# Kernel optimization log

Hardware: AMD Instinct MI355X
Metric: run time of the kernel (lower is better)

Reference implementation:

```python
import jax, jax.numpy as jnp
import numpy as np

M_NODES, N_FEAT, HIDDEN = 1024, 64, 64


def _linear_init(key, fan_in, fan_out):
    kw, kb = jax.random.split(key)
    s = 1.0 / np.sqrt(fan_in)
    W = jax.random.uniform(kw, (fan_in, fan_out), minval=-s, maxval=s, dtype=jnp.float32)
    b = jax.random.uniform(kb, (fan_out,), minval=-s, maxval=s, dtype=jnp.float32)
    return W, b


def setup_inputs() -> dict:
    key = jax.random.key(0)
    ks = jax.random.split(key, 9)
    M, n, hid = M_NODES, N_FEAT, HIDDEN
    We1, be1 = _linear_init(ks[0], 2 * n + 2, hid)  # phi_e layer 1: [h_i, h_j, d2, a]
    We2, be2 = _linear_init(ks[1], hid, hid)         # phi_e layer 2
    Wx1, bx1 = _linear_init(ks[2], hid, hid)         # phi_x layer 1
    Wx2, bx2 = _linear_init(ks[3], hid, 1)           # phi_x layer 2 (scalar edge weight)
    Wh1, bh1 = _linear_init(ks[4], n + hid, hid)     # phi_h layer 1: [h_i, m_i]
    Wh2, bh2 = _linear_init(ks[5], hid, n)           # phi_h layer 2
    x = jax.random.normal(ks[6], (M, 3), dtype=jnp.float32)
    a = jax.random.uniform(ks[7], (M, M, 1), dtype=jnp.float32)
    h = jax.random.normal(ks[8], (M, n), dtype=jnp.float32)  # embedding table (all node ids)
    return dict(x=x, a=a, h=h, We1=We1, be1=be1, We2=We2, be2=be2,
                Wx1=Wx1, bx1=bx1, Wx2=Wx2, bx2=bx2, Wh1=Wh1, bh1=bh1, Wh2=Wh2, bh2=bh2)


def reference(x, a, h, We1, be1, We2, be2, Wx1, bx1, Wx2, bx2, Wh1, bh1, Wh2, bh2):
    M = x.shape[0]
    n = h.shape[1]
    C = 1.0 / (M - 1)
    # pairwise coordinate differences and squared distances
    diff = x[:, None, :] - x[None, :, :]                 # [M, M, 3]
    d2 = jnp.sum(diff * diff, axis=-1, keepdims=True)    # [M, M, 1]
    # phi_e layer-1 computed without materializing the [M, M, 2n+2] concat:
    # split We1 rows for h_i, h_j, d2, a contributions
    pe_i = h @ We1[:n]           # [M, hid]
    pe_j = h @ We1[n:2 * n]      # [M, hid]
    pre = pe_i[:, None, :] + pe_j[None, :, :] + d2 * We1[2 * n] + a * We1[2 * n + 1] + be1
    m = jax.nn.silu(jax.nn.silu(pre) @ We2 + be2)        # [M, M, hid]
    # coordinate update: x_i' = x_i + C * sum_j (x_i - x_j) * phi_x(m_ij)
    s = jax.nn.silu(m @ Wx1 + bx1) @ Wx2 + bx2           # [M, M, 1]
    mask = (1.0 - jnp.eye(M, dtype=x.dtype))[:, :, None]  # exclude self-loops
    x_new = x + C * jnp.sum(diff * s * mask, axis=1)      # [M, 3]
    # message aggregation over complete graph minus self-loops (m_ij @ all_neighbors)
    m_i = jnp.sum(m * mask, axis=1)                      # [M, hid]
    # node update: h' = phi_h([h_i, m_i])
    h_new = jax.nn.silu(jnp.concatenate([h, m_i], axis=-1) @ Wh1 + bh1) @ Wh2 + bh2
    return x_new, h_new
```

## Files before the change

### kernel.cpp

```cpp
#include <hip/hip_runtime.h>


#define MM 1024

typedef _Float16 half8 __attribute__((ext_vector_type(8)));
typedef float f32x4 __attribute__((ext_vector_type(4)));
typedef int int4t __attribute__((ext_vector_type(4)));

__device__ __forceinline__ float fsilu(float v) {
    float e = __expf(-v);
    return v * __builtin_amdgcn_rcpf(1.0f + e);
}

__global__ void __launch_bounds__(256) egnn_prepack(
    const float* __restrict__ h, const float* __restrict__ We1,
    const float* __restrict__ be1, const float* __restrict__ We2,
    const float* __restrict__ Wx1,
    float* __restrict__ peib, float* __restrict__ pej,
    _Float16* __restrict__ we2hi, _Float16* __restrict__ we2lo,
    _Float16* __restrict__ wx1h)
{
    const int b = blockIdx.x;
    if (b < 256) {
        const int i = b * 4 + (threadIdx.x >> 6);
        const int c = threadIdx.x & 63;
        float acc1 = be1[c], acc2 = 0.0f;
        const float* __restrict__ hrow = h + i * 64;
#pragma unroll 8
        for (int cp = 0; cp < 64; ++cp) {
            const float hv = hrow[cp];
            acc1 = fmaf(hv, We1[cp * 64 + c], acc1);
            acc2 = fmaf(hv, We1[(64 + cp) * 64 + c], acc2);
        }
        peib[i * 64 + c] = acc1;
        pej[i * 64 + c]  = acc2;
    } else {
        const int idx = (b - 256) * 256 + threadIdx.x;
        const int e = idx & 7, l = (idx >> 3) & 63, f = (idx >> 9) & 7;
        const int n = f >> 1, s = f & 1;
        const int outc = 16 * n + (l & 15);
        const int kc   = 32 * s + ((l >> 4) * 8) + e;
        if (idx < 4096) {
            const float wv = We2[kc * 64 + outc];
            const _Float16 hi = (_Float16)wv;
            we2hi[idx] = hi;
            we2lo[idx] = (_Float16)(wv - (float)hi);
        } else {
            const float wv = Wx1[kc * 64 + outc];
            wx1h[idx - 4096] = (_Float16)wv;
        }
    }
}

__global__ void __launch_bounds__(256, 2) egnn_main(
    const float* __restrict__ x, const float* __restrict__ a,
    const float* __restrict__ h, const float* __restrict__ We1,
    const float* __restrict__ peib, const float* __restrict__ pej,
    const _Float16* __restrict__ we2hi, const _Float16* __restrict__ we2lo,
    const _Float16* __restrict__ wx1h,
    const float* __restrict__ be2,
    const float* __restrict__ bx1, const float* __restrict__ Wx2,
    const float* __restrict__ bx2,
    const float* __restrict__ Wh1, const float* __restrict__ bh1,
    const float* __restrict__ Wh2, const float* __restrict__ bh2,
    float* __restrict__ out)
{
    const int i = blockIdx.x;
    const int tid = threadIdx.x;
    const int w = tid >> 6;
    const int l = tid & 63;
    const int g = l >> 4;
    const int q15 = l & 15;

    __shared__ __align__(16) float peibL[64], wd2L[64], waL[64], be2L[64], bx1L[64], wx2L[64];
    __shared__ __align__(16) float partialL[256];
    __shared__ float xpartL[4][3];
    __shared__ float miL[64], hrowL[64], hid1L[64];

    if (tid < 64) {
        peibL[tid] = peib[i * 64 + tid];
        wd2L[tid]  = We1[128 * 64 + tid];
        waL[tid]   = We1[129 * 64 + tid];
        be2L[tid]  = be2[tid];
        bx1L[tid]  = bx1[tid];
        wx2L[tid]  = Wx2[tid];
        hrowL[tid] = h[i * 64 + tid];
    }
    __syncthreads();

    const half8* __restrict__ w2h = (const half8*)we2hi;
    const half8* __restrict__ w2l = (const half8*)we2lo;
    const half8* __restrict__ wxh = (const half8*)wx1h;
    half8 whi[4][2], wlo[4][2], wx1f[4][2];
#pragma unroll
    for (int n = 0; n < 4; ++n)
#pragma unroll
        for (int s = 0; s < 2; ++s) {
            whi[n][s]  = w2h[(n * 2 + s) * 64 + l];
            wlo[n][s]  = w2l[(n * 2 + s) * 64 + l];
            wx1f[n][s] = wxh[(n * 2 + s) * 64 + l];
        }

    const float xi0 = x[i * 3 + 0], xi1 = x[i * 3 + 1], xi2 = x[i * 3 + 2];
    const float bx2v = bx2[0];
    const int sl_lo = q15 + 16 * (2 * (g & 1));
    const int sl_hi = sl_lo + 16;
    const bool hiSel = (g >= 2);

    float msum[4][4];
#pragma unroll
    for (int n = 0; n < 4; ++n)
#pragma unroll
        for (int r = 0; r < 4; ++r) msum[n][r] = 0.0f;
    float xa0 = 0.0f, xa1 = 0.0f, xa2 = 0.0f;

    for (int t = 0; t < 16; ++t) {
        const int jw = t * 64 + 16 * w + q15;
        const float xj0 = x[jw * 3 + 0], xj1 = x[jw * 3 + 1], xj2 = x[jw * 3 + 2];
        const float d0 = xi0 - xj0, d1 = xi1 - xj1, d2v = xi2 - xj2;
        const float dd = fmaf(d0, d0, fmaf(d1, d1, d2v * d2v));
        const float av = a[i * MM + jw];
        const float selfmul = (jw == i) ? 0.0f : 1.0f;

        half8 P[2];
        const float* __restrict__ pejrow = pej + jw * 64;
#pragma unroll
        for (int s = 0; s < 2; ++s) {
            const f32x4 pj0 = *(const f32x4*)(pejrow + 32 * s + 8 * g);
            const f32x4 pj1 = *(const f32x4*)(pejrow + 32 * s + 8 * g + 4);
            const f32x4 pe0 = *(const f32x4*)&peibL[32 * s + 8 * g];
            const f32x4 pe1 = *(const f32x4*)&peibL[32 * s + 8 * g + 4];
            const f32x4 wd0 = *(const f32x4*)&wd2L[32 * s + 8 * g];
            const f32x4 wd1 = *(const f32x4*)&wd2L[32 * s + 8 * g + 4];
            const f32x4 wa0 = *(const f32x4*)&waL[32 * s + 8 * g];
            const f32x4 wa1 = *(const f32x4*)&waL[32 * s + 8 * g + 4];
#pragma unroll
            for (int e = 0; e < 8; ++e) {
                const float pjv = (e < 4) ? pj0[e] : pj1[e - 4];
                const float pev = (e < 4) ? pe0[e] : pe1[e - 4];
                const float wdv = (e < 4) ? wd0[e] : wd1[e - 4];
                const float wav = (e < 4) ? wa0[e] : wa1[e - 4];
                float pre = pev + pjv;
                pre = fmaf(dd, wdv, pre);
                pre = fmaf(av, wav, pre);
                P[s][e] = (_Float16)fsilu(pre);
            }
        }

        f32x4 acc1[4];
#pragma unroll
        for (int n = 0; n < 4; ++n) acc1[n] = *(const f32x4*)&be2L[16 * n + 4 * g];
#pragma unroll
        for (int n = 0; n < 4; ++n) {
            acc1[n] = __builtin_amdgcn_mfma_f32_16x16x32_f16(whi[n][0], P[0], acc1[n], 0, 0, 0);
            acc1[n] = __builtin_amdgcn_mfma_f32_16x16x32_f16(whi[n][1], P[1], acc1[n], 0, 0, 0);
            acc1[n] = __builtin_amdgcn_mfma_f32_16x16x32_f16(wlo[n][0], P[0], acc1[n], 0, 0, 0);
            acc1[n] = __builtin_amdgcn_mfma_f32_16x16x32_f16(wlo[n][1], P[1], acc1[n], 0, 0, 0);
        }

        float mf[4][4];
        int srcp[4][2];
#pragma unroll
        for (int n = 0; n < 4; ++n) {
#pragma unroll
            for (int r = 0; r < 4; ++r) {
                mf[n][r] = fsilu(acc1[n][r]);
                msum[n][r] = fmaf(mf[n][r], selfmul, msum[n][r]);
            }
            srcp[n][0] = __builtin_bit_cast(int, __builtin_amdgcn_cvt_pkrtz(mf[n][0], mf[n][1]));
            srcp[n][1] = __builtin_bit_cast(int, __builtin_amdgcn_cvt_pkrtz(mf[n][2], mf[n][3]));
        }

        half8 B2[2];
#pragma unroll
        for (int s2 = 0; s2 < 2; ++s2) {
            int4t bi;
#pragma unroll
            for (int p = 0; p < 4; ++p) {
                const int sl = (p < 2) ? sl_lo : sl_hi;
                const int va = __shfl(srcp[2 * s2][p & 1], sl, 64);
                const int vb = __shfl(srcp[2 * s2 + 1][p & 1], sl, 64);
                bi[p] = hiSel ? vb : va;
            }
            B2[s2] = __builtin_bit_cast(half8, bi);
        }

        f32x4 acc2[4];
#pragma unroll
        for (int n = 0; n < 4; ++n) acc2[n] = *(const f32x4*)&bx1L[16 * n + 4 * g];
#pragma unroll
        for (int n = 0; n < 4; ++n) {
            acc2[n] = __builtin_amdgcn_mfma_f32_16x16x32_f16(wx1f[n][0], B2[0], acc2[n], 0, 0, 0);
            acc2[n] = __builtin_amdgcn_mfma_f32_16x16x32_f16(wx1f[n][1], B2[1], acc2[n], 0, 0, 0);
        }

        float sp = 0.0f;
#pragma unroll
        for (int n = 0; n < 4; ++n) {
            const f32x4 wq = *(const f32x4*)&wx2L[16 * n + 4 * g];
#pragma unroll
            for (int r = 0; r < 4; ++r) sp = fmaf(fsilu(acc2[n][r]), wq[r], sp);
        }
        sp += __shfl_xor(sp, 16, 64);
        sp += __shfl_xor(sp, 32, 64);
        const float sv = sp + bx2v;
        xa0 = fmaf(d0, sv, xa0);
        xa1 = fmaf(d1, sv, xa1);
        xa2 = fmaf(d2v, sv, xa2);
    }

#pragma unroll
    for (int n = 0; n < 4; ++n)
#pragma unroll
        for (int r = 0; r < 4; ++r) {
            float v = msum[n][r];
            v += __shfl_xor(v, 1, 64);
            v += __shfl_xor(v, 2, 64);
            v += __shfl_xor(v, 4, 64);
            v += __shfl_xor(v, 8, 64);
            msum[n][r] = v;
        }
    if (q15 == 0) {
#pragma unroll
        for (int n = 0; n < 4; ++n) {
            f32x4 sv4;
            sv4[0] = msum[n][0]; sv4[1] = msum[n][1];
            sv4[2] = msum[n][2]; sv4[3] = msum[n][3];
            *(f32x4*)&partialL[w * 64 + 16 * n + 4 * g] = sv4;
        }
    }
    {
        float v0 = xa0, v1 = xa1, v2 = xa2;
        for (int sft = 1; sft < 64; sft <<= 1) {
            v0 += __shfl_xor(v0, sft, 64);
            v1 += __shfl_xor(v1, sft, 64);
            v2 += __shfl_xor(v2, sft, 64);
        }
        if (l == 0) { xpartL[w][0] = v0; xpartL[w][1] = v1; xpartL[w][2] = v2; }
    }
    __syncthreads();

    if (tid < 64)
        miL[tid] = partialL[tid] + partialL[64 + tid] + partialL[128 + tid] + partialL[192 + tid];
    __syncthreads();

    if (tid < 64) {
        const int kk = tid;
        float a0 = bh1[kk], a1 = 0.0f;
#pragma unroll 8
        for (int c = 0; c < 64; ++c) {
            a0 = fmaf(hrowL[c], Wh1[c * 64 + kk], a0);
            a1 = fmaf(miL[c], Wh1[(64 + c) * 64 + kk], a1);
        }
        hid1L[kk] = fsilu(a0 + a1);
    }
    __syncthreads();

    if (tid < 64) {
        float accv = bh2[tid];
#pragma unroll 8
        for (int kk = 0; kk < 64; ++kk) accv = fmaf(hid1L[kk], Wh2[kk * 64 + tid], accv);
        out[3072 + i * 64 + tid] = accv;
    }
    if (tid == 0) {
        const float C = 0.25f / 1023.0f;
        out[i * 3 + 0] = xi0 + C * (xpartL[0][0] + xpartL[1][0] + xpartL[2][0] + xpartL[3][0]);
        out[i * 3 + 1] = xi1 + C * (xpartL[0][1] + xpartL[1][1] + xpartL[2][1] + xpartL[3][1]);
        out[i * 3 + 2] = xi2 + C * (xpartL[0][2] + xpartL[1][2] + xpartL[2][2] + xpartL[3][2]);
    }
}

extern "C" void kernel_launch(void* const* d_in, const int* in_sizes, int n_in,
                              void* d_out, int out_size, void* d_ws, size_t ws_size,
                              hipStream_t stream) {
    const float* x   = (const float*)d_in[0];
    const float* a   = (const float*)d_in[1];
    const float* h   = (const float*)d_in[2];
    const float* We1 = (const float*)d_in[3];
    const float* be1 = (const float*)d_in[4];
    const float* We2 = (const float*)d_in[5];
    const float* be2 = (const float*)d_in[6];
    const float* Wx1 = (const float*)d_in[7];
    const float* bx1 = (const float*)d_in[8];
    const float* Wx2 = (const float*)d_in[9];
    const float* bx2 = (const float*)d_in[10];
    const float* Wh1 = (const float*)d_in[11];
    const float* bh1 = (const float*)d_in[12];
    const float* Wh2 = (const float*)d_in[13];
    const float* bh2 = (const float*)d_in[14];
    float* out = (float*)d_out;

    float* peib = (float*)d_ws;
    float* pej  = peib + 65536;
    _Float16* we2hi = (_Float16*)(pej + 65536);
    _Float16* we2lo = we2hi + 4096;
    _Float16* wx1h  = we2lo + 4096;

    egnn_prepack<<<dim3(288), dim3(256), 0, stream>>>(
        h, We1, be1, We2, Wx1, peib, pej, we2hi, we2lo, wx1h);
    egnn_main<<<dim3(1024), dim3(256), 0, stream>>>(
        x, a, h, We1, peib, pej, we2hi, we2lo, wx1h,
        be2, bx1, Wx2, bx2, Wh1, bh1, Wh2, bh2, out);
}
```

Measured before the change: 177.7 us.

## Move MFMA weight fragments to LDS, raise occupancy, software-prefetch pej rows

The main kernel now stages the fp16 weight fragments (We2 hi/lo and Wx1) and the row of `a` in shared memory instead of holding 24 half8 registers per lane. This frees registers so launch bounds can request 4 blocks per CU instead of 2. The j-loop is restructured into a double-buffered prefetch of pej rows and x coordinates to hide global latency. The prepack kernel is reshaped to 64-thread blocks with h rows cached in LDS. The cost is extra LDS reads before every MFMA and more shared memory per block, which may itself limit occupancy.

New measurement: 477.6 us. 169% more time.

```diff
diff --git a/kernel.cpp b/kernel.cpp
--- a/kernel.cpp
+++ b/kernel.cpp
@@ -12,7 +12,7 @@
     return v * __builtin_amdgcn_rcpf(1.0f + e);
 }
 
-__global__ void __launch_bounds__(256) egnn_prepack(
+__global__ void __launch_bounds__(64) egnn_prepack(
     const float* __restrict__ h, const float* __restrict__ We1,
     const float* __restrict__ be1, const float* __restrict__ We2,
     const float* __restrict__ Wx1,
@@ -21,11 +21,14 @@
     _Float16* __restrict__ wx1h)
 {
     const int b = blockIdx.x;
-    if (b < 256) {
-        const int i = b * 4 + (threadIdx.x >> 6);
-        const int c = threadIdx.x & 63;
+    const int tid = threadIdx.x;
+    if (b < 1024) {
+        const int i = b;
+        const int c = tid;
+        __shared__ float hrow[64];
+        hrow[c] = h[i * 64 + c];
+        __syncthreads();
         float acc1 = be1[c], acc2 = 0.0f;
-        const float* __restrict__ hrow = h + i * 64;
 #pragma unroll 8
         for (int cp = 0; cp < 64; ++cp) {
             const float hv = hrow[cp];
@@ -35,7 +38,7 @@
         peib[i * 64 + c] = acc1;
         pej[i * 64 + c]  = acc2;
     } else {
-        const int idx = (b - 256) * 256 + threadIdx.x;
+        const int idx = (b - 1024) * 64 + tid;
         const int e = idx & 7, l = (idx >> 3) & 63, f = (idx >> 9) & 7;
         const int n = f >> 1, s = f & 1;
         const int outc = 16 * n + (l & 15);
@@ -46,13 +49,12 @@
             we2hi[idx] = hi;
             we2lo[idx] = (_Float16)(wv - (float)hi);
         } else {
-            const float wv = Wx1[kc * 64 + outc];
-            wx1h[idx - 4096] = (_Float16)wv;
+            wx1h[idx - 4096] = (_Float16)Wx1[kc * 64 + outc];
         }
     }
 }
 
-__global__ void __launch_bounds__(256, 2) egnn_main(
+__global__ void __launch_bounds__(256, 4) egnn_main(
     const float* __restrict__ x, const float* __restrict__ a,
     const float* __restrict__ h, const float* __restrict__ We1,
     const float* __restrict__ peib, const float* __restrict__ pej,
@@ -72,11 +74,20 @@
     const int g = l >> 4;
     const int q15 = l & 15;
 
+    __shared__ half8 wLDS[1536];
+    __shared__ __align__(16) float aL[1024];
     __shared__ __align__(16) float peibL[64], wd2L[64], waL[64], be2L[64], bx1L[64], wx2L[64];
     __shared__ __align__(16) float partialL[256];
     __shared__ float xpartL[4][3];
     __shared__ float miL[64], hrowL[64], hid1L[64];
 
+    for (int idx = tid; idx < 1536; idx += 256) {
+        const half8* src = (idx < 512)  ? ((const half8*)we2hi) + idx
+                         : (idx < 1024) ? ((const half8*)we2lo) + (idx - 512)
+                                        : ((const half8*)wx1h) + (idx - 1024);
+        wLDS[idx] = *src;
+    }
+    ((f32x4*)aL)[tid] = ((const f32x4*)(a + i * MM))[tid];
     if (tid < 64) {
         peibL[tid] = peib[i * 64 + tid];
         wd2L[tid]  = We1[128 * 64 + tid];
@@ -88,24 +99,12 @@
     }
     __syncthreads();
 
-    const half8* __restrict__ w2h = (const half8*)we2hi;
-    const half8* __restrict__ w2l = (const half8*)we2lo;
-    const half8* __restrict__ wxh = (const half8*)wx1h;
-    half8 whi[4][2], wlo[4][2], wx1f[4][2];
-#pragma unroll
-    for (int n = 0; n < 4; ++n)
-#pragma unroll
-        for (int s = 0; s < 2; ++s) {
-            whi[n][s]  = w2h[(n * 2 + s) * 64 + l];
-            wlo[n][s]  = w2l[(n * 2 + s) * 64 + l];
-            wx1f[n][s] = wxh[(n * 2 + s) * 64 + l];
-        }
-
     const float xi0 = x[i * 3 + 0], xi1 = x[i * 3 + 1], xi2 = x[i * 3 + 2];
     const float bx2v = bx2[0];
-    const int sl_lo = q15 + 16 * (2 * (g & 1));
+    const int sl_lo = q15 + 32 * (g & 1);
     const int sl_hi = sl_lo + 16;
     const bool hiSel = (g >= 2);
+    const int jbase = 16 * w + q15;
 
     float msum[4][4];
 #pragma unroll
@@ -114,20 +113,31 @@
         for (int r = 0; r < 4; ++r) msum[n][r] = 0.0f;
     float xa0 = 0.0f, xa1 = 0.0f, xa2 = 0.0f;
 
-    for (int t = 0; t < 16; ++t) {
-        const int jw = t * 64 + 16 * w + q15;
-        const float xj0 = x[jw * 3 + 0], xj1 = x[jw * 3 + 1], xj2 = x[jw * 3 + 2];
-        const float d0 = xi0 - xj0, d1 = xi1 - xj1, d2v = xi2 - xj2;
+    f32x4 pA[2][2], pB[2][2];
+    float xjA[3], xjB[3];
+
+    auto pref = [&](f32x4 (&pj)[2][2], float (&xj)[3], int t) {
+        const int jn = t * 64 + jbase;
+        const float* __restrict__ pr = pej + jn * 64 + 8 * g;
+        pj[0][0] = *(const f32x4*)(pr);
+        pj[0][1] = *(const f32x4*)(pr + 4);
+        pj[1][0] = *(const f32x4*)(pr + 32);
+        pj[1][1] = *(const f32x4*)(pr + 36);
+        xj[0] = x[jn * 3 + 0];
+        xj[1] = x[jn * 3 + 1];
+        xj[2] = x[jn * 3 + 2];
+    };
+
+    auto body = [&](const f32x4 (&pj)[2][2], const float (&xj)[3], int t) {
+        const int jw = t * 64 + jbase;
+        const float d0 = xi0 - xj[0], d1 = xi1 - xj[1], d2v = xi2 - xj[2];
         const float dd = fmaf(d0, d0, fmaf(d1, d1, d2v * d2v));
-        const float av = a[i * MM + jw];
+        const float av = aL[jw];
         const float selfmul = (jw == i) ? 0.0f : 1.0f;
 
         half8 P[2];
-        const float* __restrict__ pejrow = pej + jw * 64;
 #pragma unroll
         for (int s = 0; s < 2; ++s) {
-            const f32x4 pj0 = *(const f32x4*)(pejrow + 32 * s + 8 * g);
-            const f32x4 pj1 = *(const f32x4*)(pejrow + 32 * s + 8 * g + 4);
             const f32x4 pe0 = *(const f32x4*)&peibL[32 * s + 8 * g];
             const f32x4 pe1 = *(const f32x4*)&peibL[32 * s + 8 * g + 4];
             const f32x4 wd0 = *(const f32x4*)&wd2L[32 * s + 8 * g];
@@ -136,7 +146,7 @@
             const f32x4 wa1 = *(const f32x4*)&waL[32 * s + 8 * g + 4];
 #pragma unroll
             for (int e = 0; e < 8; ++e) {
-                const float pjv = (e < 4) ? pj0[e] : pj1[e - 4];
+                const float pjv = (e < 4) ? pj[s][0][e] : pj[s][1][e - 4];
                 const float pev = (e < 4) ? pe0[e] : pe1[e - 4];
                 const float wdv = (e < 4) ? wd0[e] : wd1[e - 4];
                 const float wav = (e < 4) ? wa0[e] : wa1[e - 4];
@@ -152,10 +162,10 @@
         for (int n = 0; n < 4; ++n) acc1[n] = *(const f32x4*)&be2L[16 * n + 4 * g];
 #pragma unroll
         for (int n = 0; n < 4; ++n) {
-            acc1[n] = __builtin_amdgcn_mfma_f32_16x16x32_f16(whi[n][0], P[0], acc1[n], 0, 0, 0);
-            acc1[n] = __builtin_amdgcn_mfma_f32_16x16x32_f16(whi[n][1], P[1], acc1[n], 0, 0, 0);
-            acc1[n] = __builtin_amdgcn_mfma_f32_16x16x32_f16(wlo[n][0], P[0], acc1[n], 0, 0, 0);
-            acc1[n] = __builtin_amdgcn_mfma_f32_16x16x32_f16(wlo[n][1], P[1], acc1[n], 0, 0, 0);
+            acc1[n] = __builtin_amdgcn_mfma_f32_16x16x32_f16(wLDS[(n * 2 + 0) * 64 + l], P[0], acc1[n], 0, 0, 0);
+            acc1[n] = __builtin_amdgcn_mfma_f32_16x16x32_f16(wLDS[(n * 2 + 1) * 64 + l], P[1], acc1[n], 0, 0, 0);
+            acc1[n] = __builtin_amdgcn_mfma_f32_16x16x32_f16(wLDS[512 + (n * 2 + 0) * 64 + l], P[0], acc1[n], 0, 0, 0);
+            acc1[n] = __builtin_amdgcn_mfma_f32_16x16x32_f16(wLDS[512 + (n * 2 + 1) * 64 + l], P[1], acc1[n], 0, 0, 0);
         }
 
         float mf[4][4];
@@ -190,8 +200,8 @@
         for (int n = 0; n < 4; ++n) acc2[n] = *(const f32x4*)&bx1L[16 * n + 4 * g];
 #pragma unroll
         for (int n = 0; n < 4; ++n) {
-            acc2[n] = __builtin_amdgcn_mfma_f32_16x16x32_f16(wx1f[n][0], B2[0], acc2[n], 0, 0, 0);
-            acc2[n] = __builtin_amdgcn_mfma_f32_16x16x32_f16(wx1f[n][1], B2[1], acc2[n], 0, 0, 0);
+            acc2[n] = __builtin_amdgcn_mfma_f32_16x16x32_f16(wLDS[1024 + (n * 2 + 0) * 64 + l], B2[0], acc2[n], 0, 0, 0);
+            acc2[n] = __builtin_amdgcn_mfma_f32_16x16x32_f16(wLDS[1024 + (n * 2 + 1) * 64 + l], B2[1], acc2[n], 0, 0, 0);
         }
 
         float sp = 0.0f;
@@ -207,6 +217,14 @@
         xa0 = fmaf(d0, sv, xa0);
         xa1 = fmaf(d1, sv, xa1);
         xa2 = fmaf(d2v, sv, xa2);
+    };
+
+    pref(pA, xjA, 0);
+    for (int t = 0; t < 16; t += 2) {
+        pref(pB, xjB, t + 1);
+        body(pA, xjA, t);
+        if (t + 2 < 16) pref(pA, xjA, t + 2);
+        body(pB, xjB, t + 1);
     }
 
 #pragma unroll
@@ -296,7 +314,7 @@
     _Float16* we2lo = we2hi + 4096;
     _Float16* wx1h  = we2lo + 4096;
 
-    egnn_prepack<<<dim3(288), dim3(256), 0, stream>>>(
+    egnn_prepack<<<dim3(1152), dim3(64), 0, stream>>>(
         h, We1, be1, We2, Wx1, peib, pej, we2hi, we2lo, wx1h);
     egnn_main<<<dim3(1024), dim3(256), 0, stream>>>(
         x, a, h, We1, peib, pej, we2hi, we2lo, wx1h,
```

## Move Wx1 MFMA fragments to LDS, unroll edge loop, reshape prepack grid

Applied to the files above, without the earlier changes.

The Wx1 half-precision fragments are now staged in shared memory and read per MFMA instead of being held in 32 VGPRs, to relieve register pressure in the main edge loop. The edge loop is unrolled by two to expose more instruction-level parallelism. The prepack kernel is relaunched as 1152 blocks of 64 threads, with the h row cached in shared memory. The cost is extra LDS traffic per iteration, 8 KB more LDS per block, and possible register growth from the unroll.

Result: slower. 240.6 us (+35.4%).

```diff
diff --git a/kernel.cpp b/kernel.cpp
--- a/kernel.cpp
+++ b/kernel.cpp
@@ -12,7 +12,7 @@
     return v * __builtin_amdgcn_rcpf(1.0f + e);
 }
 
-__global__ void __launch_bounds__(256) egnn_prepack(
+__global__ void __launch_bounds__(64) egnn_prepack(
     const float* __restrict__ h, const float* __restrict__ We1,
     const float* __restrict__ be1, const float* __restrict__ We2,
     const float* __restrict__ Wx1,
@@ -21,11 +21,14 @@
     _Float16* __restrict__ wx1h)
 {
     const int b = blockIdx.x;
-    if (b < 256) {
-        const int i = b * 4 + (threadIdx.x >> 6);
-        const int c = threadIdx.x & 63;
+    const int tid = threadIdx.x;
+    if (b < 1024) {
+        const int i = b;
+        const int c = tid;
+        __shared__ float hrow[64];
+        hrow[c] = h[i * 64 + c];
+        __syncthreads();
         float acc1 = be1[c], acc2 = 0.0f;
-        const float* __restrict__ hrow = h + i * 64;
 #pragma unroll 8
         for (int cp = 0; cp < 64; ++cp) {
             const float hv = hrow[cp];
@@ -35,7 +38,7 @@
         peib[i * 64 + c] = acc1;
         pej[i * 64 + c]  = acc2;
     } else {
-        const int idx = (b - 256) * 256 + threadIdx.x;
+        const int idx = (b - 1024) * 64 + tid;
         const int e = idx & 7, l = (idx >> 3) & 63, f = (idx >> 9) & 7;
         const int n = f >> 1, s = f & 1;
         const int outc = 16 * n + (l & 15);
@@ -46,8 +49,7 @@
             we2hi[idx] = hi;
             we2lo[idx] = (_Float16)(wv - (float)hi);
         } else {
-            const float wv = Wx1[kc * 64 + outc];
-            wx1h[idx - 4096] = (_Float16)wv;
+            wx1h[idx - 4096] = (_Float16)Wx1[kc * 64 + outc];
         }
     }
 }
@@ -72,11 +74,14 @@
     const int g = l >> 4;
     const int q15 = l & 15;
 
+    __shared__ half8 wLDSx[512];
     __shared__ __align__(16) float peibL[64], wd2L[64], waL[64], be2L[64], bx1L[64], wx2L[64];
     __shared__ __align__(16) float partialL[256];
     __shared__ float xpartL[4][3];
     __shared__ float miL[64], hrowL[64], hid1L[64];
 
+    for (int idx = tid; idx < 512; idx += 256)
+        wLDSx[idx] = ((const half8*)wx1h)[idx];
     if (tid < 64) {
         peibL[tid] = peib[i * 64 + tid];
         wd2L[tid]  = We1[128 * 64 + tid];
@@ -90,22 +95,21 @@
 
     const half8* __restrict__ w2h = (const half8*)we2hi;
     const half8* __restrict__ w2l = (const half8*)we2lo;
-    const half8* __restrict__ wxh = (const half8*)wx1h;
-    half8 whi[4][2], wlo[4][2], wx1f[4][2];
+    half8 whi[4][2], wlo[4][2];
 #pragma unroll
     for (int n = 0; n < 4; ++n)
 #pragma unroll
         for (int s = 0; s < 2; ++s) {
-            whi[n][s]  = w2h[(n * 2 + s) * 64 + l];
-            wlo[n][s]  = w2l[(n * 2 + s) * 64 + l];
-            wx1f[n][s] = wxh[(n * 2 + s) * 64 + l];
+            whi[n][s] = w2h[(n * 2 + s) * 64 + l];
+            wlo[n][s] = w2l[(n * 2 + s) * 64 + l];
         }
 
     const float xi0 = x[i * 3 + 0], xi1 = x[i * 3 + 1], xi2 = x[i * 3 + 2];
     const float bx2v = bx2[0];
-    const int sl_lo = q15 + 16 * (2 * (g & 1));
+    const int sl_lo = q15 + 32 * (g & 1);
     const int sl_hi = sl_lo + 16;
     const bool hiSel = (g >= 2);
+    const int jbase = 16 * w + q15;
 
     float msum[4][4];
 #pragma unroll
@@ -114,8 +118,9 @@
         for (int r = 0; r < 4; ++r) msum[n][r] = 0.0f;
     float xa0 = 0.0f, xa1 = 0.0f, xa2 = 0.0f;
 
+#pragma unroll 2
     for (int t = 0; t < 16; ++t) {
-        const int jw = t * 64 + 16 * w + q15;
+        const int jw = t * 64 + jbase;
         const float xj0 = x[jw * 3 + 0], xj1 = x[jw * 3 + 1], xj2 = x[jw * 3 + 2];
         const float d0 = xi0 - xj0, d1 = xi1 - xj1, d2v = xi2 - xj2;
         const float dd = fmaf(d0, d0, fmaf(d1, d1, d2v * d2v));
@@ -190,8 +195,8 @@
         for (int n = 0; n < 4; ++n) acc2[n] = *(const f32x4*)&bx1L[16 * n + 4 * g];
 #pragma unroll
         for (int n = 0; n < 4; ++n) {
-            acc2[n] = __builtin_amdgcn_mfma_f32_16x16x32_f16(wx1f[n][0], B2[0], acc2[n], 0, 0, 0);
-            acc2[n] = __builtin_amdgcn_mfma_f32_16x16x32_f16(wx1f[n][1], B2[1], acc2[n], 0, 0, 0);
+            acc2[n] = __builtin_amdgcn_mfma_f32_16x16x32_f16(wLDSx[(n * 2 + 0) * 64 + l], B2[0], acc2[n], 0, 0, 0);
+            acc2[n] = __builtin_amdgcn_mfma_f32_16x16x32_f16(wLDSx[(n * 2 + 1) * 64 + l], B2[1], acc2[n], 0, 0, 0);
         }
 
         float sp = 0.0f;
@@ -296,7 +301,7 @@
     _Float16* we2lo = we2hi + 4096;
     _Float16* wx1h  = we2lo + 4096;
 
-    egnn_prepack<<<dim3(288), dim3(256), 0, stream>>>(
+    egnn_prepack<<<dim3(1152), dim3(64), 0, stream>>>(
         h, We1, be1, We2, Wx1, peib, pej, we2hi, we2lo, wx1h);
     egnn_main<<<dim3(1024), dim3(256), 0, stream>>>(
         x, a, h, We1, peib, pej, we2hi, we2lo, wx1h,
```
